# Kernel tuning notes

Measured on AMD Instinct MI355X. Metric: run time of the kernel, lower is better.

The kernel has to match this reference:

```python
import jax, jax.numpy as jnp
import numpy as np

P, C, H, W = 512, 32, 64, 48   # instances, channels, heatmap size
PDIM = 34                      # 17 keypoints * 2 coords
NUM_IMAGES = 32
NORM_FACT = 96.0               # cfg.DATASET.OUTPUT_SIZE
PARAM_NORM = 480.0


def setup_inputs() -> dict:
    key = jax.random.key(0)
    k1, k2, k3 = jax.random.split(key, 3)
    instance_feats = jax.random.normal(k1, (P, C, H, W), dtype=jnp.float32)
    imgid = jnp.sort(jax.random.randint(k2, (P,), 0, NUM_IMAGES))  # consecutive groups
    instance_param = jax.random.normal(k3, (P, PDIM), dtype=jnp.float32)
    return {"instance_feats": instance_feats, "imgid": imgid,
            "instance_param": instance_param, "j": 0}


def reference(instance_feats, imgid, instance_param, j):
    # instance_feats: [P, C, H, W]; imgid: [P] (sorted -> consecutive groups)
    p, c, h, w = instance_feats.shape
    x = instance_feats.transpose(1, 0, 2, 3).reshape(c, p, h * w)  # [C, P, HW]

    # Per-pair relation. The original computes this per ragged group; since the
    # softmax is over the CHANNEL axis (dim=0), pairs do not interact, so we can
    # compute all pairs densely and mask cross-group pairs before the value matmul.
    rel = jnp.einsum('cid,cjd->cij', x, x) / NORM_FACT            # [C, P, P]
    rel = rel + (instance_param @ instance_param.T) / PARAM_NORM  # broadcast [P, P]
    att = jax.nn.softmax(rel, axis=0)                              # softmax over channels

    same_img = (imgid[:, None] == imgid[None, :]).astype(x.dtype)  # [P, P] group mask
    out = jnp.einsum('cij,cjd->cid', att * same_img[None], x)      # [C, P, HW]

    out = out.reshape(c, p, h, w).transpose(1, 0, 2, 3) + instance_feats
    return jax.nn.relu(out)
```

## Files before the change

### kernel.cpp

```cpp
#include <hip/hip_runtime.h>
#include <hip/hip_bf16.h>

#define PP   512
#define CC   32
#define HWD  3072
#define PDIMK 34
#define NIMG 32
#define NCH  (HWD / 256)

static constexpr float INV_NORM  = 1.0f / 96.0f;
static constexpr float INV_PNORM = 1.0f / 480.0f;

typedef short bf16x8 __attribute__((ext_vector_type(8)));
typedef float f32x4  __attribute__((ext_vector_type(4)));

__device__ __forceinline__ short f2bf(float f) {
    __hip_bfloat16 h = __float2bfloat16(f);
    return *reinterpret_cast<short*>(&h);
}

__device__ __forceinline__ void gload_lds16(const float* g, float* l) {
    __builtin_amdgcn_global_load_lds(
        (const __attribute__((address_space(1))) void*)g,
        (__attribute__((address_space(3))) void*)l, 16, 0, 0);
}


__global__ void k_groups(const int* __restrict__ imgid, int* __restrict__ wsI) {
    __shared__ int s_img[PP];
    __shared__ int s_cnt[PP];
    int t = threadIdx.x;
    s_img[t] = imgid[t];
    __syncthreads();
    int v = s_img[t];
    int lo = 0, hi = PP;
    while (lo < hi) { int mid = (lo + hi) >> 1; if (s_img[mid] < v) lo = mid + 1; else hi = mid; }
    int st = lo;
    lo = 0; hi = PP;
    while (lo < hi) { int mid = (lo + hi) >> 1; if (s_img[mid] <= v) lo = mid + 1; else hi = mid; }
    int cn = lo - st;
    wsI[64 + t]  = st;
    wsI[576 + t] = cn;
    s_cnt[t] = cn;
    if (t <= NIMG) {
        lo = 0; hi = PP;
        while (lo < hi) { int mid = (lo + hi) >> 1; if (s_img[mid] < t) lo = mid + 1; else hi = mid; }
        wsI[t] = lo;
    }
    __syncthreads();
    if (t == 0) {
        int acc = 0;
        for (int i = 0; i < PP; ++i) { wsI[1088 + i] = acc; acc += s_cnt[i]; }
        wsI[33] = acc;
    }
}

__global__ __launch_bounds__(256) void k_rel(const float* __restrict__ feats,
                                             const int* __restrict__ wsI,
                                             float* __restrict__ relbuf, int strideP) {
    __shared__ float buf[2][32 * 256];
    __shared__ f32x4 red[3][4][64];
    int m = blockIdx.x, c = blockIdx.y;
    int g0 = wsI[m], n = wsI[m + 1] - g0;
    if (n <= 0) return;
    const int* pairBase = wsI + 1088;
    int t = threadIdx.x, wave = t >> 6, lane = t & 63;
    int fr = lane & 15, fq = lane >> 4;
    const size_t rstride = (size_t)CC * HWD;
    const float* base = feats + ((size_t)g0 * CC + c) * HWD;
    int nt = (n + 15) >> 4;
    int s = fr & 7;

    if (nt == 1) {
        f32x4 acc = {0.f, 0.f, 0.f, 0.f};
        for (int rr = 0; rr < 4; ++rr) {
            int r = wave * 4 + rr;
            if (r < n) gload_lds16(base + (size_t)r * rstride + ((lane ^ (r & 7)) << 2),
                                   &buf[0][r * 256]);
        }
        __syncthreads();
        for (int ch = 0; ch < NCH; ++ch) {
            int cur = ch & 1;
            if (ch + 1 < NCH) {
                int kc = (ch + 1) * 256;
                for (int rr = 0; rr < 4; ++rr) {
                    int r = wave * 4 + rr;
                    if (r < n) gload_lds16(base + (size_t)r * rstride + kc + ((lane ^ (r & 7)) << 2),
                                           &buf[cur ^ 1][r * 256]);
                }
            }
#pragma unroll
            for (int k2 = 0; k2 < 2; ++k2) {
                int q0 = (wave * 2 + k2) * 8 + fq * 2;
                float4 f0 = *(const float4*)&buf[cur][fr * 256 + ((q0 ^ s) << 2)];
                float4 f1 = *(const float4*)&buf[cur][fr * 256 + (((q0 + 1) ^ s) << 2)];
                bf16x8 af = { f2bf(f0.x), f2bf(f0.y), f2bf(f0.z), f2bf(f0.w),
                              f2bf(f1.x), f2bf(f1.y), f2bf(f1.z), f2bf(f1.w) };
                acc = __builtin_amdgcn_mfma_f32_16x16x32_bf16(af, af, acc, 0, 0, 0);
            }
            __syncthreads();
        }
        red[0][wave][lane] = acc;
        __syncthreads();
        if (wave == 0) {
            f32x4 s4 = red[0][0][lane] + red[0][1][lane] + red[0][2][lane] + red[0][3][lane];
#pragma unroll
            for (int q = 0; q < 4; ++q) {
                int i = fq * 4 + q, j = fr;
                if (i < n && j < n) {
                    int p = pairBase[g0 + i] + j;
                    if (p < strideP) relbuf[(size_t)c * strideP + p] = s4[q] * INV_NORM;
                }
            }
        }
    } else if (nt == 2) {
        f32x4 a00 = {0.f,0.f,0.f,0.f}, a01 = a00, a11 = a00;
        for (int rr = 0; rr < 8; ++rr) {
            int r = wave * 8 + rr;
            if (r < n) gload_lds16(base + (size_t)r * rstride + ((lane ^ (r & 7)) << 2),
                                   &buf[0][r * 256]);
        }
        __syncthreads();
        for (int ch = 0; ch < NCH; ++ch) {
            int cur = ch & 1;
            if (ch + 1 < NCH) {
                int kc = (ch + 1) * 256;
                for (int rr = 0; rr < 8; ++rr) {
                    int r = wave * 8 + rr;
                    if (r < n) gload_lds16(base + (size_t)r * rstride + kc + ((lane ^ (r & 7)) << 2),
                                           &buf[cur ^ 1][r * 256]);
                }
            }
#pragma unroll
            for (int k2 = 0; k2 < 2; ++k2) {
                int q0 = (wave * 2 + k2) * 8 + fq * 2;
                float4 u0 = *(const float4*)&buf[cur][fr * 256 + ((q0 ^ s) << 2)];
                float4 u1 = *(const float4*)&buf[cur][fr * 256 + (((q0 + 1) ^ s) << 2)];
                float4 v0 = *(const float4*)&buf[cur][(16 + fr) * 256 + ((q0 ^ s) << 2)];
                float4 v1 = *(const float4*)&buf[cur][(16 + fr) * 256 + (((q0 + 1) ^ s) << 2)];
                bf16x8 af = { f2bf(u0.x), f2bf(u0.y), f2bf(u0.z), f2bf(u0.w),
                              f2bf(u1.x), f2bf(u1.y), f2bf(u1.z), f2bf(u1.w) };
                bf16x8 bf = { f2bf(v0.x), f2bf(v0.y), f2bf(v0.z), f2bf(v0.w),
                              f2bf(v1.x), f2bf(v1.y), f2bf(v1.z), f2bf(v1.w) };
                a00 = __builtin_amdgcn_mfma_f32_16x16x32_bf16(af, af, a00, 0, 0, 0);
                a01 = __builtin_amdgcn_mfma_f32_16x16x32_bf16(af, bf, a01, 0, 0, 0);
                a11 = __builtin_amdgcn_mfma_f32_16x16x32_bf16(bf, bf, a11, 0, 0, 0);
            }
            __syncthreads();
        }
        red[0][wave][lane] = a00;
        red[1][wave][lane] = a01;
        red[2][wave][lane] = a11;
        __syncthreads();
        if (wave < 3) {
            f32x4 s4 = red[wave][0][lane] + red[wave][1][lane] +
                       red[wave][2][lane] + red[wave][3][lane];
#pragma unroll
            for (int q = 0; q < 4; ++q) {
                int il = fq * 4 + q, jl = fr;
                int i = (wave == 2) ? 16 + il : il;
                int j = (wave == 0) ? jl : 16 + jl;
                if (i < n && j < n) {
                    int p = pairBase[g0 + i] + j;
                    if (p < strideP) relbuf[(size_t)c * strideP + p] = s4[q] * INV_NORM;
                    if (wave == 1) {
                        int p2 = pairBase[g0 + j] + i;
                        if (p2 < strideP) relbuf[(size_t)c * strideP + p2] = s4[q] * INV_NORM;
                    }
                }
            }
        }
    } else {
        for (int ti = 0; ti < nt; ++ti)
            for (int tj = ti; tj < nt; ++tj) {
                bool diag = (ti == tj);
                f32x4 acc = {0.f, 0.f, 0.f, 0.f};
                for (int ch = 0; ch < NCH; ++ch) {
                    int kc = ch * 256;
                    __syncthreads();
                    for (int rr = 0; rr < 4; ++rr) {
                        int rl = wave * 4 + rr;
                        int rgi = ti * 16 + rl;
                        if (rgi < n) gload_lds16(base + (size_t)rgi * rstride + kc + ((lane ^ (rl & 7)) << 2),
                                                 &buf[0][rl * 256]);
                        if (!diag) {
                            int rgj = tj * 16 + rl;
                            if (rgj < n) gload_lds16(base + (size_t)rgj * rstride + kc + ((lane ^ (rl & 7)) << 2),
                                                     &buf[0][(16 + rl) * 256]);
                        }
                    }
                    __syncthreads();
#pragma unroll
                    for (int k2 = 0; k2 < 2; ++k2) {
                        int q0 = (wave * 2 + k2) * 8 + fq * 2;
                        float4 u0 = *(const float4*)&buf[0][fr * 256 + ((q0 ^ s) << 2)];
                        float4 u1 = *(const float4*)&buf[0][fr * 256 + (((q0 + 1) ^ s) << 2)];
                        bf16x8 af = { f2bf(u0.x), f2bf(u0.y), f2bf(u0.z), f2bf(u0.w),
                                      f2bf(u1.x), f2bf(u1.y), f2bf(u1.z), f2bf(u1.w) };
                        bf16x8 bf = af;
                        if (!diag) {
                            float4 v0 = *(const float4*)&buf[0][(16 + fr) * 256 + ((q0 ^ s) << 2)];
                            float4 v1 = *(const float4*)&buf[0][(16 + fr) * 256 + (((q0 + 1) ^ s) << 2)];
                            bf16x8 bb = { f2bf(v0.x), f2bf(v0.y), f2bf(v0.z), f2bf(v0.w),
                                          f2bf(v1.x), f2bf(v1.y), f2bf(v1.z), f2bf(v1.w) };
                            bf = bb;
                        }
                        acc = __builtin_amdgcn_mfma_f32_16x16x32_bf16(af, bf, acc, 0, 0, 0);
                    }
                }
                __syncthreads();
                red[0][wave][lane] = acc;
                __syncthreads();
                if (wave == 0) {
                    f32x4 s4 = red[0][0][lane] + red[0][1][lane] + red[0][2][lane] + red[0][3][lane];
#pragma unroll
                    for (int q = 0; q < 4; ++q) {
                        int i = ti * 16 + fq * 4 + q, j = tj * 16 + fr;
                        if (i < n && j < n) {
                            int p = pairBase[g0 + i] + j;
                            if (p < strideP) relbuf[(size_t)c * strideP + p] = s4[q] * INV_NORM;
                            if (!diag) {
                                int p2 = pairBase[g0 + j] + i;
                                if (p2 < strideP) relbuf[(size_t)c * strideP + p2] = s4[q] * INV_NORM;
                            }
                        }
                    }
                }
                __syncthreads();
            }
    }
}

__global__ __launch_bounds__(256) void k_softmax(float* __restrict__ relbuf,
                                                 const float* __restrict__ param,
                                                 const int* __restrict__ wsI, int strideP) {
    int np = wsI[33];
    if (np > strideP) np = strideP;
    int p0 = blockIdx.x * 64;
    if (p0 >= np) return;
    int nv = min(64, np - p0);
    __shared__ float tile[CC][68];
    int t = threadIdx.x;
    for (int idx = t; idx < CC * 16; idx += 256) {
        int c = idx >> 4, q4 = (idx & 15) * 4;
        if (q4 + 4 <= nv) {
            *(float4*)&tile[c][q4] = *(const float4*)&relbuf[(size_t)c * strideP + p0 + q4];
        } else {
#pragma unroll
            for (int e = 0; e < 4; ++e)
                if (q4 + e < nv) tile[c][q4 + e] = relbuf[(size_t)c * strideP + p0 + q4 + e];
        }
    }
    __syncthreads();
    if (t < 64 && t < nv) {
        int p = p0 + t;
        const int* pairBase = wsI + 1088;
        int lo = 0, hi = PP - 1;
        while (lo < hi) { int mid = (lo + hi + 1) >> 1; if (pairBase[mid] <= p) lo = mid; else hi = mid - 1; }
        int i = lo;
        int j = wsI[64 + i] + (p - pairBase[i]);
        float pd = 0.f;
#pragma unroll
        for (int k = 0; k < PDIMK; ++k) pd += param[i * PDIMK + k] * param[j * PDIMK + k];
        pd *= INV_PNORM;
        float mx = -3.4e38f;
#pragma unroll
        for (int c = 0; c < CC; ++c) mx = fmaxf(mx, tile[c][t] + pd);
        float ssum = 0.f;
#pragma unroll
        for (int c = 0; c < CC; ++c) { float e = __expf(tile[c][t] + pd - mx); tile[c][t] = e; ssum += e; }
        float inv = 1.0f / ssum;
#pragma unroll
        for (int c = 0; c < CC; ++c) tile[c][t] *= inv;
    }
    __syncthreads();
    for (int idx = t; idx < CC * 16; idx += 256) {
        int c = idx >> 4, q4 = (idx & 15) * 4;
        if (q4 + 4 <= nv) {
            *(float4*)&relbuf[(size_t)c * strideP + p0 + q4] = *(const float4*)&tile[c][q4];
        } else {
#pragma unroll
            for (int e = 0; e < 4; ++e)
                if (q4 + e < nv) relbuf[(size_t)c * strideP + p0 + q4 + e] = tile[c][q4 + e];
        }
    }
}

__global__ __launch_bounds__(256) void k_out(const float* __restrict__ feats,
                                             const float* __restrict__ att,
                                             const int* __restrict__ wsI,
                                             float* __restrict__ out, int strideP) {
    __shared__ float att_t[32][20];
    int m = blockIdx.x, c = blockIdx.y;
    int g0 = wsI[m], n = wsI[m + 1] - g0;
    if (n <= 0) return;
    const int* pairBase = wsI + 1088;
    int t = threadIdx.x;
    int col = blockIdx.z * 1024 + t * 4;
    const size_t rs = (size_t)CC * HWD;
    const float* fb = feats + ((size_t)g0 * CC + c) * HWD + col;
    float*       ob = out   + ((size_t)g0 * CC + c) * HWD + col;

    for (int ic = 0; ic < n; ic += 16) {
        int ni = min(16, n - ic);
        float4 acc[16];
#pragma unroll
        for (int q = 0; q < 16; ++q) acc[q] = make_float4(0.f, 0.f, 0.f, 0.f);
        for (int jc = 0; jc < n; jc += 32) {
            int nj = min(32, n - jc);
            __syncthreads();
            for (int idx = t; idx < 512; idx += 256) {
                int jj = idx & 31, ii = idx >> 5;
                float a = 0.f;
                if (ii < ni && jj < nj) {
                    int p = pairBase[g0 + ic + ii] + jc + jj;
                    if (p < strideP) a = att[(size_t)c * strideP + p];
                    if (ic + ii == jc + jj) a += 1.0f;
                }
                att_t[jj][ii] = a;
            }
            __syncthreads();
            const float* fj = fb + (size_t)jc * rs;
            float4 vnext = *(const float4*)fj;
            for (int jj = 0; jj < nj; ++jj) {
                float4 vj = vnext;
                if (jj + 1 < nj) vnext = *(const float4*)(fj + (size_t)(jj + 1) * rs);
                float4 a0 = *(const float4*)&att_t[jj][0];
                float4 a1 = *(const float4*)&att_t[jj][4];
                float4 a2 = *(const float4*)&att_t[jj][8];
                float4 a3 = *(const float4*)&att_t[jj][12];
                acc[0].x  += a0.x * vj.x; acc[0].y  += a0.x * vj.y; acc[0].z  += a0.x * vj.z; acc[0].w  += a0.x * vj.w;
                acc[1].x  += a0.y * vj.x; acc[1].y  += a0.y * vj.y; acc[1].z  += a0.y * vj.z; acc[1].w  += a0.y * vj.w;
                acc[2].x  += a0.z * vj.x; acc[2].y  += a0.z * vj.y; acc[2].z  += a0.z * vj.z; acc[2].w  += a0.z * vj.w;
                acc[3].x  += a0.w * vj.x; acc[3].y  += a0.w * vj.y; acc[3].z  += a0.w * vj.z; acc[3].w  += a0.w * vj.w;
                acc[4].x  += a1.x * vj.x; acc[4].y  += a1.x * vj.y; acc[4].z  += a1.x * vj.z; acc[4].w  += a1.x * vj.w;
                acc[5].x  += a1.y * vj.x; acc[5].y  += a1.y * vj.y; acc[5].z  += a1.y * vj.z; acc[5].w  += a1.y * vj.w;
                acc[6].x  += a1.z * vj.x; acc[6].y  += a1.z * vj.y; acc[6].z  += a1.z * vj.z; acc[6].w  += a1.z * vj.w;
                acc[7].x  += a1.w * vj.x; acc[7].y  += a1.w * vj.y; acc[7].z  += a1.w * vj.z; acc[7].w  += a1.w * vj.w;
                acc[8].x  += a2.x * vj.x; acc[8].y  += a2.x * vj.y; acc[8].z  += a2.x * vj.z; acc[8].w  += a2.x * vj.w;
                acc[9].x  += a2.y * vj.x; acc[9].y  += a2.y * vj.y; acc[9].z  += a2.y * vj.z; acc[9].w  += a2.y * vj.w;
                acc[10].x += a2.z * vj.x; acc[10].y += a2.z * vj.y; acc[10].z += a2.z * vj.z; acc[10].w += a2.z * vj.w;
                acc[11].x += a2.w * vj.x; acc[11].y += a2.w * vj.y; acc[11].z += a2.w * vj.z; acc[11].w += a2.w * vj.w;
                acc[12].x += a3.x * vj.x; acc[12].y += a3.x * vj.y; acc[12].z += a3.x * vj.z; acc[12].w += a3.x * vj.w;
                acc[13].x += a3.y * vj.x; acc[13].y += a3.y * vj.y; acc[13].z += a3.y * vj.z; acc[13].w += a3.y * vj.w;
                acc[14].x += a3.z * vj.x; acc[14].y += a3.z * vj.y; acc[14].z += a3.z * vj.z; acc[14].w += a3.z * vj.w;
                acc[15].x += a3.w * vj.x; acc[15].y += a3.w * vj.y; acc[15].z += a3.w * vj.z; acc[15].w += a3.w * vj.w;
            }
        }
#pragma unroll
        for (int ii = 0; ii < 16; ++ii) {
            if (ii < ni) {
                float4 r = acc[ii];
                r.x = fmaxf(r.x, 0.f); r.y = fmaxf(r.y, 0.f);
                r.z = fmaxf(r.z, 0.f); r.w = fmaxf(r.w, 0.f);
                *(float4*)&ob[(size_t)(ic + ii) * rs] = r;
            }
        }
    }
}

extern "C" void kernel_launch(void* const* d_in, const int* in_sizes, int n_in,
                              void* d_out, int out_size, void* d_ws, size_t ws_size,
                              hipStream_t stream) {
    const float* feats = (const float*)d_in[0];
    const int*   imgid = (const int*)d_in[1];
    const float* param = (const float*)d_in[2];
    float* out = (float*)d_out;
    int* wsI = (int*)d_ws;
    float* relbuf = (float*)((char*)d_ws + 8192);

    long capL = ((long)ws_size - 8192) / (CC * 4);
    if (capL < 0) capL = 0;
    if (capL > (long)PP * PP) capL = (long)PP * PP;
    int strideP = (int)capL;

    k_groups<<<1, PP, 0, stream>>>(imgid, wsI);
    k_rel<<<dim3(NIMG, CC), 256, 0, stream>>>(feats, wsI, relbuf, strideP);
    k_softmax<<<dim3((PP * PP + 63) / 64), 256, 0, stream>>>(relbuf, param, wsI, strideP);
    k_out<<<dim3(NIMG, CC, 3), 256, 0, stream>>>(feats, relbuf, wsI, out, strideP);
}
```

Baseline: 164.8 us.

## Restructure k_out to stage group features in LDS with finer column tiling

```diff
diff --git a/kernel.cpp b/kernel.cpp
--- a/kernel.cpp
+++ b/kernel.cpp
@@ -290,71 +290,83 @@
                                              const float* __restrict__ att,
                                              const int* __restrict__ wsI,
                                              float* __restrict__ out, int strideP) {
-    __shared__ float att_t[32][20];
-    int m = blockIdx.x, c = blockIdx.y;
+    __shared__ float X[32][256];
+    __shared__ float att_s[32][36];
+    int m = blockIdx.x, c = blockIdx.y, z = blockIdx.z;
     int g0 = wsI[m], n = wsI[m + 1] - g0;
     if (n <= 0) return;
     const int* pairBase = wsI + 1088;
-    int t = threadIdx.x;
-    int col = blockIdx.z * 1024 + t * 4;
+    int t = threadIdx.x, wave = t >> 6, lane = t & 63;
     const size_t rs = (size_t)CC * HWD;
-    const float* fb = feats + ((size_t)g0 * CC + c) * HWD + col;
-    float*       ob = out   + ((size_t)g0 * CC + c) * HWD + col;
-
-    for (int ic = 0; ic < n; ic += 16) {
-        int ni = min(16, n - ic);
-        float4 acc[16];
-#pragma unroll
-        for (int q = 0; q < 16; ++q) acc[q] = make_float4(0.f, 0.f, 0.f, 0.f);
-        for (int jc = 0; jc < n; jc += 32) {
-            int nj = min(32, n - jc);
-            __syncthreads();
-            for (int idx = t; idx < 512; idx += 256) {
-                int jj = idx & 31, ii = idx >> 5;
-                float a = 0.f;
-                if (ii < ni && jj < nj) {
-                    int p = pairBase[g0 + ic + ii] + jc + jj;
-                    if (p < strideP) a = att[(size_t)c * strideP + p];
-                    if (ic + ii == jc + jj) a += 1.0f;
-                }
-                att_t[jj][ii] = a;
-            }
-            __syncthreads();
-            const float* fj = fb + (size_t)jc * rs;
-            float4 vnext = *(const float4*)fj;
-            for (int jj = 0; jj < nj; ++jj) {
-                float4 vj = vnext;
-                if (jj + 1 < nj) vnext = *(const float4*)(fj + (size_t)(jj + 1) * rs);
-                float4 a0 = *(const float4*)&att_t[jj][0];
-                float4 a1 = *(const float4*)&att_t[jj][4];
-                float4 a2 = *(const float4*)&att_t[jj][8];
-                float4 a3 = *(const float4*)&att_t[jj][12];
-                acc[0].x  += a0.x * vj.x; acc[0].y  += a0.x * vj.y; acc[0].z  += a0.x * vj.z; acc[0].w  += a0.x * vj.w;
-                acc[1].x  += a0.y * vj.x; acc[1].y  += a0.y * vj.y; acc[1].z  += a0.y * vj.z; acc[1].w  += a0.y * vj.w;
-                acc[2].x  += a0.z * vj.x; acc[2].y  += a0.z * vj.y; acc[2].z  += a0.z * vj.z; acc[2].w  += a0.z * vj.w;
-                acc[3].x  += a0.w * vj.x; acc[3].y  += a0.w * vj.y; acc[3].z  += a0.w * vj.z; acc[3].w  += a0.w * vj.w;
-                acc[4].x  += a1.x * vj.x; acc[4].y  += a1.x * vj.y; acc[4].z  += a1.x * vj.z; acc[4].w  += a1.x * vj.w;
-                acc[5].x  += a1.y * vj.x; acc[5].y  += a1.y * vj.y; acc[5].z  += a1.y * vj.z; acc[5].w  += a1.y * vj.w;
-                acc[6].x  += a1.z * vj.x; acc[6].y  += a1.z * vj.y; acc[6].z  += a1.z * vj.z; acc[6].w  += a1.z * vj.w;
-                acc[7].x  += a1.w * vj.x; acc[7].y  += a1.w * vj.y; acc[7].z  += a1.w * vj.z; acc[7].w  += a1.w * vj.w;
-                acc[8].x  += a2.x * vj.x; acc[8].y  += a2.x * vj.y; acc[8].z  += a2.x * vj.z; acc[8].w  += a2.x * vj.w;
-                acc[9].x  += a2.y * vj.x; acc[9].y  += a2.y * vj.y; acc[9].z  += a2.y * vj.z; acc[9].w  += a2.y * vj.w;
-                acc[10].x += a2.z * vj.x; acc[10].y += a2.z * vj.y; acc[10].z += a2.z * vj.z; acc[10].w += a2.z * vj.w;
-                acc[11].x += a2.w * vj.x; acc[11].y += a2.w * vj.y; acc[11].z += a2.w * vj.z; acc[11].w += a2.w * vj.w;
-                acc[12].x += a3.x * vj.x; acc[12].y += a3.x * vj.y; acc[12].z += a3.x * vj.z; acc[12].w += a3.x * vj.w;
-                acc[13].x += a3.y * vj.x; acc[13].y += a3.y * vj.y; acc[13].z += a3.y * vj.z; acc[13].w += a3.y * vj.w;
-                acc[14].x += a3.z * vj.x; acc[14].y += a3.z * vj.y; acc[14].z += a3.z * vj.z; acc[14].w += a3.z * vj.w;
-                acc[15].x += a3.w * vj.x; acc[15].y += a3.w * vj.y; acc[15].z += a3.w * vj.z; acc[15].w += a3.w * vj.w;
-            }
-        }
-#pragma unroll
-        for (int ii = 0; ii < 16; ++ii) {
-            if (ii < ni) {
-                float4 r = acc[ii];
+    const float* base = feats + ((size_t)g0 * CC + c) * HWD + z * 256;
+    float*       ob   = out   + ((size_t)g0 * CC + c) * HWD + z * 256;
+
+    if (n <= 32) {
+        for (int r = wave; r < n; r += 4)
+            gload_lds16(base + (size_t)r * rs + lane * 4, &X[r][0]);
+        int nn = n * n;
+        float av[4] = {0.f, 0.f, 0.f, 0.f};
+#pragma unroll
+        for (int q = 0; q < 4; ++q) {
+            int idx = t + q * 256;
+            if (idx < nn) {
+                int ii = idx / n, jj = idx - ii * n;
+                int p = pairBase[g0 + ii] + jj;
+                if (p < strideP) av[q] = att[(size_t)c * strideP + p];
+                if (ii == jj) av[q] += 1.0f;
+            }
+        }
+        for (int idx = t; idx < 32 * 36; idx += 256) (&att_s[0][0])[idx] = 0.f;
+        __syncthreads();
+#pragma unroll
+        for (int q = 0; q < 4; ++q) {
+            int idx = t + q * 256;
+            if (idx < nn) { int ii = idx / n, jj = idx - ii * n; att_s[ii][jj] = av[q]; }
+        }
+        int nz = (n + 3) & ~3; if (nz > 32) nz = 32;
+        for (int r = n + wave; r < nz; r += 4)
+            *(float4*)&X[r][lane * 4] = make_float4(0.f, 0.f, 0.f, 0.f);
+        __syncthreads();
+        float4 acc[8];
+#pragma unroll
+        for (int k = 0; k < 8; ++k) acc[k] = make_float4(0.f, 0.f, 0.f, 0.f);
+        for (int j0 = 0; j0 < n; j0 += 4) {
+            float4 xj0 = *(const float4*)&X[j0][lane * 4];
+            float4 xj1 = *(const float4*)&X[j0 + 1][lane * 4];
+            float4 xj2 = *(const float4*)&X[j0 + 2][lane * 4];
+            float4 xj3 = *(const float4*)&X[j0 + 3][lane * 4];
+#pragma unroll
+            for (int k = 0; k < 8; ++k) {
+                int i = wave + 4 * k;
+                if (i < n) {
+                    float4 a4 = *(const float4*)&att_s[i][j0];
+                    acc[k].x += a4.x * xj0.x + a4.y * xj1.x + a4.z * xj2.x + a4.w * xj3.x;
+                    acc[k].y += a4.x * xj0.y + a4.y * xj1.y + a4.z * xj2.y + a4.w * xj3.y;
+                    acc[k].z += a4.x * xj0.z + a4.y * xj1.z + a4.z * xj2.z + a4.w * xj3.z;
+                    acc[k].w += a4.x * xj0.w + a4.y * xj1.w + a4.z * xj2.w + a4.w * xj3.w;
+                }
+            }
+        }
+#pragma unroll
+        for (int k = 0; k < 8; ++k) {
+            int i = wave + 4 * k;
+            if (i < n) {
+                float4 r = acc[k];
                 r.x = fmaxf(r.x, 0.f); r.y = fmaxf(r.y, 0.f);
                 r.z = fmaxf(r.z, 0.f); r.w = fmaxf(r.w, 0.f);
-                *(float4*)&ob[(size_t)(ic + ii) * rs] = r;
-            }
+                *(float4*)&ob[(size_t)i * rs + lane * 4] = r;
+            }
+        }
+    } else {
+        for (int ii = 0; ii < n; ++ii) {
+            long pb = pairBase[g0 + ii];
+            float accv = 0.f;
+            for (int jj = 0; jj < n; ++jj) {
+                float a = (pb + jj < strideP) ? att[(size_t)c * strideP + pb + jj] : 0.f;
+                if (ii == jj) a += 1.0f;
+                accv += a * base[(size_t)jj * rs + t];
+            }
+            ob[(size_t)ii * rs + t] = fmaxf(accv, 0.f);
         }
     }
 }
@@ -377,5 +389,5 @@
     k_groups<<<1, PP, 0, stream>>>(imgid, wsI);
     k_rel<<<dim3(NIMG, CC), 256, 0, stream>>>(feats, wsI, relbuf, strideP);
     k_softmax<<<dim3((PP * PP + 63) / 64), 256, 0, stream>>>(relbuf, param, wsI, strideP);
-    k_out<<<dim3(NIMG, CC, 3), 256, 0, stream>>>(feats, relbuf, wsI, out, strideP);
-}
+    k_out<<<dim3(NIMG, CC, NCH), 256, 0, stream>>>(feats, relbuf, wsI, out, strideP);
+}
```

Measured after the change: 172.9 us. 4.9% more time.
